# Optimization experiments

Hardware: AMD Instinct MI355X
Metric: run time of the kernel (lower is better)

Reference implementation:

```python
import jax, jax.numpy as jnp
import numpy as np

N_NODES = 10000
NUM_GENE = 2000
N_EDGES = 160000
HEADS = 10
HID = 128          # GAT layer1 out_channels
LATENT = 128
LOWER = 64
CLUSTERS = 15
SIGMA = 0.5
NEG_SLOPE = 0.2


def gat_conv(x, src, dst, W, a_src, a_dst, b, concat):
    """PyG GATConv (eval mode, self-loops already appended to src/dst).
    x: [N, Fin]; W: [Fin, H*D]; a_src/a_dst: [H, D]; b: [H*D] or [D]."""
    N = x.shape[0]
    H, D = a_src.shape
    h = (x @ W).reshape(N, H, D)                       # [N,H,D]
    e_s = jnp.einsum('nhd,hd->nh', h, a_src)           # [N,H]
    e_d = jnp.einsum('nhd,hd->nh', h, a_dst)
    alpha = jax.nn.leaky_relu(e_s[src] + e_d[dst], NEG_SLOPE)   # [E,H]
    m = jax.ops.segment_max(alpha, dst, num_segments=N)          # [N,H]
    p = jnp.exp(alpha - m[dst])
    s = jax.ops.segment_sum(p, dst, num_segments=N)
    w = p / s[dst]                                     # segment softmax [E,H]
    out = jax.ops.segment_sum(h[src] * w[:, :, None], dst, num_segments=N)  # [N,H,D]
    out = out.reshape(N, H * D) if concat else out.mean(axis=1)
    return out + b


def add_self_loops(edge_index, n):
    loop = jnp.arange(n, dtype=edge_index.dtype)
    src = jnp.concatenate([edge_index[0], loop])
    dst = jnp.concatenate([edge_index[1], loop])
    return src, dst


def setup_inputs() -> dict:
    key = jax.random.key(0)
    ks = jax.random.split(key, 20)
    g = lambda k, shape, fan: jax.random.normal(k, shape, jnp.float32) * (1.0 / np.sqrt(fan))
    inp = {
        'x': jax.random.normal(ks[0], (N_NODES, NUM_GENE), jnp.float32),
        'edge_index': jax.random.randint(ks[1], (2, N_EDGES), 0, N_NODES, dtype=jnp.int32),
        'noise': jax.random.normal(ks[2], (N_NODES, NUM_GENE), jnp.float32) * SIGMA,
        # GAT layer 1: in=NUM_GENE, out=HID, heads=HEADS, concat
        'W1': g(ks[3], (NUM_GENE, HEADS * HID), NUM_GENE),
        'a1_src': g(ks[4], (HEADS, HID), HID),
        'a1_dst': g(ks[5], (HEADS, HID), HID),
        'b1': jnp.zeros((HEADS * HID,), jnp.float32),
        # GAT layer 2: in=HEADS*HID, out=LATENT, heads=HEADS, mean
        'W2': g(ks[6], (HEADS * HID, HEADS * LATENT), HEADS * HID),
        'a2_src': g(ks[7], (HEADS, LATENT), LATENT),
        'a2_dst': g(ks[8], (HEADS, LATENT), LATENT),
        'b2': jnp.zeros((LATENT,), jnp.float32),
        # MLP
        'Wm1': g(ks[9], (NUM_GENE, LATENT), NUM_GENE),
        'bm1': jnp.zeros((LATENT,), jnp.float32),
        'Wm2': g(ks[10], (LATENT, LATENT), LATENT),
        'bm2': jnp.zeros((LATENT,), jnp.float32),
        # projection heads
        'Wf': g(ks[11], (LATENT, LOWER), LATENT),
        'bf': jnp.zeros((LOWER,), jnp.float32),
        'Wc': g(ks[12], (LATENT, CLUSTERS), LATENT),
        'bc': jnp.zeros((CLUSTERS,), jnp.float32),
    }
    return inp


def reference(x, edge_index, noise, W1, a1_src, a1_dst, b1, W2, a2_src, a2_dst, b2,
              Wm1, bm1, Wm2, bm2, Wf, bf, Wc, bc):
    N = x.shape[0]
    src, dst = add_self_loops(edge_index, N)

    # x_aug = x + F.normalize(noise, dim=1)
    nrm = jnp.sqrt(jnp.sum(noise * noise, axis=1, keepdims=True))
    x_aug = x + noise / jnp.maximum(nrm, 1e-12)

    def gat_enc(inp):
        h1 = jax.nn.relu(gat_conv(inp, src, dst, W1, a1_src, a1_dst, b1, concat=True))
        h2 = jax.nn.relu(gat_conv(h1, src, dst, W2, a2_src, a2_dst, b2, concat=False))
        return h2

    gx = gat_enc(x)          # [N, LATENT]
    gx1 = gat_enc(x_aug)
    gx2 = (jax.nn.relu(x @ Wm1 + bm1)) @ Wm2 + bm2   # MLP

    g0 = gx.mean(axis=0)     # global avg pooling -> [LATENT]
    g1 = gx1.mean(axis=0)
    g2 = gx2.mean(axis=0)

    T = 0.2
    e01 = jnp.exp(jnp.dot(g0, g1) / T)
    e02 = jnp.exp(jnp.dot(g0, g2) / T)
    e12 = jnp.exp(jnp.dot(g1, g2) / T)
    loss_graph = -jnp.log10(e01 / (e01 + e02 + e12))

    gx_node = gx @ Wf + bf
    gx1_node = gx1 @ Wf + bf
    gx2_node = gx2 @ Wf + bf
    gx_c = (gx @ Wc + bc).T      # [CLUSTERS, N]
    gx1_c = (gx1 @ Wc + bc).T
    return (gx_node, gx1_node, gx2_node, loss_graph, gx_c, gx1_c)
```

## Files before the change

### kernel.cpp

```cpp
#include <hip/hip_runtime.h>
#include <hip/hip_bf16.h>

#define N_NODESC 10000
#define M_PAD    10112
#define RT_TILES 79
#define NUM_GENE 2000
#define KPAD_G   2048
#define N_EDGESC 160000
#define E_TOT    170000
#define HEADS    10
#define F1       1280
#define LATENTC  128
#define LOWERC   64
#define CLUST    15

typedef __attribute__((ext_vector_type(8))) short   short8;
typedef __attribute__((ext_vector_type(4))) float   f32x4;
typedef __attribute__((ext_vector_type(4))) unsigned short ushort4_;

__device__ __forceinline__ float bf2f(unsigned short u){
    unsigned int x = ((unsigned int)u) << 16;
    return __builtin_bit_cast(float, x);
}
__device__ __forceinline__ unsigned short f2bf(float f){
    __hip_bfloat16 h = __float2bfloat16(f);
    return __builtin_bit_cast(unsigned short, h);
}
__device__ __forceinline__ void gload16(const void* g, void* l) {
    __builtin_amdgcn_global_load_lds((const __attribute__((address_space(1))) void*)g,
                                     (__attribute__((address_space(3))) void*)l, 16, 0, 0);
}

template<int OMODE, int FOLD>
__global__ __launch_bounds__(512, 2)
void gemm256(const unsigned short* __restrict__ A, int lda,
             const unsigned short* __restrict__ BT, int ldb,
             void* __restrict__ Cp, int ldc,
             int NK, int NT, int M_real,
             const float* __restrict__ mbias, unsigned short* __restrict__ mout)
{
    __shared__ short smem[65536];

    const int nwg = gridDim.x;
    const int q = nwg >> 3, r = nwg & 7;
    const int xcd = blockIdx.x & 7, idx = blockIdx.x >> 3;
    const int wgid = (xcd < r ? xcd * (q + 1) : r * (q + 1) + (xcd - r) * q) + idx;
    const int bm = wgid / NT, bn = wgid - bm * NT;

    const int t = threadIdx.x, w = t >> 6, lane = t & 63;
    const int wr2 = (w >> 2) * 64;
    const int wc2 = (w & 3) * 32;
    const int lrow = lane & 15, lq = lane >> 4;

    int rowc[2], swc[2], loff[2];
    #pragma unroll
    for (int cc = 0; cc < 2; ++cc) {
        int c = cc * 512 + t;
        int row = c >> 3, slot = c & 7;
        rowc[cc] = row;
        swc[cc]  = (slot ^ (row & 7)) << 3;
        loff[cc] = c * 8;
    }
    auto stageA = [&](int buf, int h, int kt) {
        short* dst = smem + buf * 32768 + h * 8192;
        const unsigned short* src = A + (size_t)(bm * 256 + h * 128) * lda + kt * 64;
        #pragma unroll
        for (int cc = 0; cc < 2; ++cc)
            gload16(src + (size_t)rowc[cc] * lda + swc[cc], dst + loff[cc]);
    };
    auto stageB = [&](int buf, int h, int kt) {
        short* dst = smem + buf * 32768 + 16384 + h * 8192;
        const unsigned short* src = BT + (size_t)(bn * 256 + h * 128) * ldb + kt * 64;
        #pragma unroll
        for (int cc = 0; cc < 2; ++cc)
            gload16(src + (size_t)rowc[cc] * ldb + swc[cc], dst + loff[cc]);
    };
    auto rdA = [&](int buf, int h, int mi, int ks) -> short8 {
        int r7 = wr2 + mi * 16 + lrow;
        return *(const short8*)(smem + buf * 32768 + h * 8192 + r7 * 64
                                + (((ks * 4 + lq) ^ (r7 & 7)) << 3));
    };
    auto rdB = [&](int buf, int h, int ni, int ks) -> short8 {
        int r7 = wc2 + ni * 16 + lrow;
        return *(const short8*)(smem + buf * 32768 + 16384 + h * 8192 + r7 * 64
                                + (((ks * 4 + lq) ^ (r7 & 7)) << 3));
    };

    f32x4 acc00[4][2] = {}, acc01[4][2] = {}, acc10[4][2] = {}, acc11[4][2] = {};
    short8 a0[4][2], a1[4][2], b0[2][2], b1[2][2];

    auto domfma = [&](f32x4 (&ac)[4][2], short8 (&aa)[4][2], short8 (&bb)[2][2]) {
        __builtin_amdgcn_s_setprio(1);
        #pragma unroll
        for (int mi = 0; mi < 4; ++mi)
            #pragma unroll
            for (int ni = 0; ni < 2; ++ni)
                #pragma unroll
                for (int ks = 0; ks < 2; ++ks)
                    ac[mi][ni] = __builtin_amdgcn_mfma_f32_16x16x32_bf16(
                        aa[mi][ks], bb[ni][ks], ac[mi][ni], 0, 0, 0);
        __builtin_amdgcn_s_setprio(0);
    };

    stageA(0, 0, 0); stageB(0, 0, 0); stageB(0, 1, 0); stageA(0, 1, 0);

    for (int kt = 0; kt < NK; ++kt) {
        const int buf = kt & 1, nbuf = buf ^ 1;
        const bool pf = (kt + 1 < NK);
        asm volatile("s_waitcnt vmcnt(4)" ::: "memory");
        __builtin_amdgcn_sched_barrier(0);
        __builtin_amdgcn_s_barrier();
        __builtin_amdgcn_sched_barrier(0);
        #pragma unroll
        for (int mi = 0; mi < 4; ++mi) { a0[mi][0] = rdA(buf, 0, mi, 0); a0[mi][1] = rdA(buf, 0, mi, 1); }
        #pragma unroll
        for (int ni = 0; ni < 2; ++ni) { b0[ni][0] = rdB(buf, 0, ni, 0); b0[ni][1] = rdB(buf, 0, ni, 1); }
        if (pf) stageA(nbuf, 0, kt + 1);
        domfma(acc00, a0, b0);
        if (pf) { asm volatile("s_waitcnt vmcnt(4)" ::: "memory"); }
        else    { asm volatile("s_waitcnt vmcnt(2)" ::: "memory"); }
        __builtin_amdgcn_sched_barrier(0);
        __builtin_amdgcn_s_barrier();
        __builtin_amdgcn_sched_barrier(0);
        #pragma unroll
        for (int ni = 0; ni < 2; ++ni) { b1[ni][0] = rdB(buf, 1, ni, 0); b1[ni][1] = rdB(buf, 1, ni, 1); }
        if (pf) stageB(nbuf, 0, kt + 1);
        domfma(acc01, a0, b1);
        if (pf) { asm volatile("s_waitcnt vmcnt(4)" ::: "memory"); }
        else    { asm volatile("s_waitcnt vmcnt(0)" ::: "memory"); }
        __builtin_amdgcn_sched_barrier(0);
        __builtin_amdgcn_s_barrier();
        __builtin_amdgcn_sched_barrier(0);
        #pragma unroll
        for (int mi = 0; mi < 4; ++mi) { a1[mi][0] = rdA(buf, 1, mi, 0); a1[mi][1] = rdA(buf, 1, mi, 1); }
        if (pf) stageB(nbuf, 1, kt + 1);
        domfma(acc10, a1, b0);
        if (pf) stageA(nbuf, 1, kt + 1);
        domfma(acc11, a1, b1);
    }

    const bool mlp_tile = FOLD && (bn == NT - 1);
    #pragma unroll
    for (int qa = 0; qa < 2; ++qa) {
        #pragma unroll
        for (int qb = 0; qb < 2; ++qb) {
            f32x4 (&ac)[4][2] = (qa == 0) ? (qb == 0 ? acc00 : acc01)
                                          : (qb == 0 ? acc10 : acc11);
            if (mlp_tile) {
                if (qb != 0) continue;
                #pragma unroll
                for (int mi = 0; mi < 4; ++mi) {
                    #pragma unroll
                    for (int ni = 0; ni < 2; ++ni) {
                        int col = wc2 + ni * 16 + lrow;
                        #pragma unroll
                        for (int qq = 0; qq < 4; ++qq) {
                            int grow = bm * 256 + qa * 128 + wr2 + mi * 16 + lq * 4 + qq;
                            if (grow < N_NODESC) {
                                float val = fmaxf(ac[mi][ni][qq] + mbias[col], 0.f);
                                mout[(size_t)grow * 128 + col] = f2bf(val);
                            }
                        }
                    }
                }
                continue;
            }
            #pragma unroll
            for (int mi = 0; mi < 4; ++mi) {
                #pragma unroll
                for (int ni = 0; ni < 2; ++ni) {
                    int gcol = bn * 256 + qb * 128 + wc2 + ni * 16 + lrow;
                    #pragma unroll
                    for (int qq = 0; qq < 4; ++qq) {
                        int grow = bm * 256 + qa * 128 + wr2 + mi * 16 + lq * 4 + qq;
                        float val = ac[mi][ni][qq];
                        int rslab = grow >= M_PAD ? grow - M_PAD : grow;
                        if (rslab >= M_real) val = 0.f;
                        if constexpr (OMODE == 0)
                            ((unsigned short*)Cp)[(size_t)grow * ldc + gcol] = f2bf(val);
                        else
                            ((float*)Cp)[(size_t)grow * ldc + gcol] = val;
                    }
                }
            }
        }
    }
}

template<int OMODE, int BIAS, int RELU>
__global__ __launch_bounds__(256)
void gemm2(const unsigned short* __restrict__ A, int lda,
           const unsigned short* __restrict__ BT, int ldb,
           const float* __restrict__ bias,
           void* __restrict__ Cp, int ldc,
           int KT, int NT, int M_real)
{
    __shared__ short smem[16384];

    const int nwg = gridDim.x;
    const int q = nwg >> 3, r = nwg & 7;
    const int xcd = blockIdx.x & 7, idx = blockIdx.x >> 3;
    const int wgid = (xcd < r ? xcd * (q + 1) : r * (q + 1) + (xcd - r) * q) + idx;
    const int bm = wgid / NT, bn = wgid - bm * NT;

    const int t = threadIdx.x, w = t >> 6, lane = t & 63;
    const int wr = (w >> 1) * 64, wc = (w & 1) * 64;
    const int lrow = lane & 15, lq = lane >> 4;

    const unsigned short* Ag[2];
    const unsigned short* Bg[2];
    int lds_off[2];
    #pragma unroll
    for (int cc = 0; cc < 2; ++cc) {
        int c = cc * 256 + t;
        int row = c >> 2, slot = c & 3;
        int gk = (slot ^ ((row >> 1) & 3)) << 3;
        Ag[cc] = A  + (size_t)(bm * 128 + row) * lda + gk;
        Bg[cc] = BT + (size_t)(bn * 128 + row) * ldb + gk;
        lds_off[cc] = cc * 2048 + w * 512 + lane * 8;
    }

    auto stage = [&](int buf, int kt) {
        const int kk = kt * 32;
        #pragma unroll
        for (int cc = 0; cc < 2; ++cc) {
            gload16(Ag[cc] + kk, smem + buf * 8192 + lds_off[cc]);
            gload16(Bg[cc] + kk, smem + buf * 8192 + 4096 + lds_off[cc]);
        }
    };

    f32x4 acc[4][4] = {};
    stage(0, 0);
    __syncthreads();
    int cur = 0;
    for (int kt = 0; kt < KT; ++kt) {
        if (kt + 1 < KT) stage(cur ^ 1, kt + 1);
        const short* As = smem + cur * 8192;
        const short* Bs = As + 4096;
        short8 af[4], bf_[4];
        #pragma unroll
        for (int mi = 0; mi < 4; ++mi) {
            int rr = wr + mi * 16 + lrow;
            af[mi] = *(const short8*)(&As[rr * 32 + ((lq ^ ((rr >> 1) & 3)) << 3)]);
        }
        #pragma unroll
        for (int ni = 0; ni < 4; ++ni) {
            int rr = wc + ni * 16 + lrow;
            bf_[ni] = *(const short8*)(&Bs[rr * 32 + ((lq ^ ((rr >> 1) & 3)) << 3)]);
        }
        #pragma unroll
        for (int mi = 0; mi < 4; ++mi)
            #pragma unroll
            for (int ni = 0; ni < 4; ++ni)
                acc[mi][ni] = __builtin_amdgcn_mfma_f32_16x16x32_bf16(af[mi], bf_[ni], acc[mi][ni], 0, 0, 0);
        __syncthreads();
        cur ^= 1;
    }

    #pragma unroll
    for (int mi = 0; mi < 4; ++mi) {
        #pragma unroll
        for (int ni = 0; ni < 4; ++ni) {
            int gcol = bn * 128 + wc + ni * 16 + lrow;
            #pragma unroll
            for (int qq = 0; qq < 4; ++qq) {
                int grow = bm * 128 + wr + mi * 16 + lq * 4 + qq;
                float val = acc[mi][ni][qq];
                if constexpr (BIAS) val += bias[gcol];
                if constexpr (RELU) val = fmaxf(val, 0.f);
                if (grow >= M_real) val = 0.f;
                ((float*)Cp)[(size_t)grow * ldc + gcol] = val;
            }
        }
    }
}

__global__ void convert_both_k(const float* __restrict__ x, const float* __restrict__ noise,
                               unsigned short* __restrict__ out)
{
    __shared__ float sred[4];
    __shared__ float srn;
    int row = blockIdx.x, t = threadIdx.x;
    int kc = t * 8;
    f32x4 n0 = {}, n1 = {};
    float ss = 0.f;
    if (t < 250) {
        n0 = *(const f32x4*)(noise + (size_t)row * NUM_GENE + kc);
        n1 = *(const f32x4*)(noise + (size_t)row * NUM_GENE + kc + 4);
        ss = n0.x*n0.x + n0.y*n0.y + n0.z*n0.z + n0.w*n0.w
           + n1.x*n1.x + n1.y*n1.y + n1.z*n1.z + n1.w*n1.w;
    }
    for (int off = 32; off; off >>= 1) ss += __shfl_down(ss, off);
    if ((t & 63) == 0) sred[t >> 6] = ss;
    __syncthreads();
    if (t == 0) srn = 1.f / fmaxf(sqrtf(sred[0] + sred[1] + sred[2] + sred[3]), 1e-12f);
    __syncthreads();
    if (t >= 250) return;
    float rn = srn;
    f32x4 a0 = *(const f32x4*)(x + (size_t)row * NUM_GENE + kc);
    f32x4 a1 = *(const f32x4*)(x + (size_t)row * NUM_GENE + kc + 4);
    short8 v0, v1;
    #pragma unroll
    for (int i = 0; i < 4; ++i) {
        v0[i]     = (short)f2bf(a0[i]);
        v0[4 + i] = (short)f2bf(a1[i]);
        v1[i]     = (short)f2bf(a0[i] + n0[i] * rn);
        v1[4 + i] = (short)f2bf(a1[i] + n1[i] * rn);
    }
    *(short8*)(out + (size_t)row * KPAD_G + kc) = v0;
    *(short8*)(out + (size_t)(M_PAD + row) * KPAD_G + kc) = v1;
}

__global__ void transpose_bf_k(const float* __restrict__ in, unsigned short* __restrict__ out,
                               int R, int C, int Kpad)
{
    __shared__ float tile[32][33];
    int tx = threadIdx.x & 31, ty = threadIdx.x >> 5;
    int c0 = blockIdx.x * 32, r0 = blockIdx.y * 32;
    #pragma unroll
    for (int i = 0; i < 4; ++i) {
        int r = r0 + ty + i * 8, c = c0 + tx;
        tile[ty + i * 8][tx] = (r < R && c < C) ? in[(size_t)r * C + c] : 0.f;
    }
    __syncthreads();
    #pragma unroll
    for (int i = 0; i < 4; ++i) {
        int c = c0 + ty + i * 8;
        int r = r0 + tx;
        if (c < C && r < Kpad) out[(size_t)c * Kpad + r] = f2bf(tile[tx][ty + i * 8]);
    }
}

__global__ void hist_k(const int* __restrict__ ei, int* __restrict__ cnt)
{
    int e = blockIdx.x * 256 + threadIdx.x;
    if (e >= E_TOT) return;
    int d = (e < N_EDGESC) ? ei[N_EDGESC + e] : (e - N_EDGESC);
    atomicAdd(&cnt[d], 1);
}

__global__ void scan_k(const int* __restrict__ cnt, int* __restrict__ rowp, int* __restrict__ cursor)
{
    __shared__ int buf[1024];
    int t = threadIdx.x;
    int loc[10];
    int s = 0, base = t * 10;
    #pragma unroll
    for (int i = 0; i < 10; ++i) {
        int idx = base + i;
        int v = (idx < N_NODESC) ? cnt[idx] : 0;
        loc[i] = v; s += v;
    }
    buf[t] = s; __syncthreads();
    for (int off = 1; off < 1024; off <<= 1) {
        int tmp = (t >= off) ? buf[t - off] : 0;
        __syncthreads();
        buf[t] += tmp;
        __syncthreads();
    }
    int run = buf[t] - s;
    #pragma unroll
    for (int i = 0; i < 10; ++i) {
        int idx = base + i;
        if (idx < N_NODESC) { rowp[idx] = run; cursor[idx] = run; run += loc[i]; }
    }
    if (t == 1023) rowp[N_NODESC] = buf[1023];
}

__global__ void scatter_k(const int* __restrict__ ei, int* __restrict__ cursor,
                          int* __restrict__ col_src, int* __restrict__ dst_of)
{
    int e = blockIdx.x * 256 + threadIdx.x;
    if (e >= E_TOT) return;
    int s, d;
    if (e < N_EDGESC) { s = ei[e]; d = ei[N_EDGESC + e]; } else { s = d = e - N_EDGESC; }
    int pos = atomicAdd(&cursor[d], 1);
    col_src[pos] = s;
    dst_of[pos] = d;
}

__global__ void escores2_k(const unsigned short* __restrict__ h,
                           const float* __restrict__ a_src, const float* __restrict__ a_dst,
                           float* __restrict__ e_s, float* __restrict__ e_d)
{
    int t = threadIdx.x;
    int half = (t >= 160);
    int tl = t - half * 160;
    int node2 = blockIdx.x * 2 + half;
    int p = node2 >= N_NODESC;
    int n = node2 - p * N_NODESC;
    int hh = tl >> 4, c = tl & 15;
    int off = hh * 128 + c * 8;
    short8 v = *(const short8*)(h + (size_t)(p * M_PAD + n) * F1 + off);
    float ps = 0.f, pd = 0.f;
    #pragma unroll
    for (int j = 0; j < 8; ++j) {
        float f = bf2f((unsigned short)v[j]);
        ps += f * a_src[off + j];
        pd += f * a_dst[off + j];
    }
    #pragma unroll
    for (int m = 1; m < 16; m <<= 1) {
        ps += __shfl_xor(ps, m, 16);
        pd += __shfl_xor(pd, m, 16);
    }
    if (c == 0) { e_s[node2 * HEADS + hh] = ps; e_d[node2 * HEADS + hh] = pd; }
}

__global__ void alpha_k(const int* __restrict__ colsrc, const int* __restrict__ dstof,
                        const float* __restrict__ e_s, const float* __restrict__ e_d,
                        float* __restrict__ alpha)
{
    int gid = blockIdx.x * 256 + threadIdx.x;
    if (gid >= 2 * E_TOT) return;
    int p = gid >= E_TOT;
    int e = gid - p * E_TOT;
    int s = colsrc[e], d = dstof[e];
    const float* er = e_s + (size_t)(p * N_NODESC + s) * HEADS;
    const float* dr = e_d + (size_t)(p * N_NODESC + d) * HEADS;
    #pragma unroll
    for (int h = 0; h < HEADS; ++h) {
        float a = er[h] + dr[h];
        a = a >= 0.f ? a : 0.2f * a;
        alpha[((size_t)p * HEADS + h) * E_TOT + e] = a;
    }
}

__global__ void nodems_k(const int* __restrict__ rowp, const float* __restrict__ alpha,
                         float2* __restrict__ minv)
{
    int gid = blockIdx.x * 256 + threadIdx.x;
    if (gid >= 2 * N_NODESC * HEADS) return;
    int p = gid >= N_NODESC * HEADS;
    int rr = gid - p * N_NODESC * HEADS;
    int n = rr / HEADS, hh = rr - n * HEADS;
    int beg = rowp[n], end = rowp[n + 1];
    const float* ap = alpha + ((size_t)p * HEADS + hh) * E_TOT;
    float m = -1e30f, ssum = 0.f;
    for (int e = beg; e < end; ++e) {
        float a = ap[e];
        if (a > m) { ssum = ssum * __expf(m - a) + 1.f; m = a; }
        else ssum += __expf(a - m);
    }
    float2 qo; qo.x = m; qo.y = 1.f / ssum;
    minv[gid] = qo;
}

__global__ void wexp_k(const int* __restrict__ dstof, const float2* __restrict__ minv,
                       float* __restrict__ alpha)
{
    int gid = blockIdx.x * 256 + threadIdx.x;
    if (gid >= 2 * E_TOT) return;
    int p = gid >= E_TOT;
    int e = gid - p * E_TOT;
    int d = dstof[e];
    const float2* mv = minv + (size_t)(p * N_NODESC + d) * HEADS;
    #pragma unroll
    for (int h = 0; h < HEADS; ++h) {
        float2 qv = mv[h];
        size_t o = ((size_t)p * HEADS + h) * E_TOT + e;
        alpha[o] = __expf(alpha[o] - qv.x) * qv.y;
    }
}

template<int L1MODE>
__global__ void agg_slice_k(const int* __restrict__ rowp, const int* __restrict__ colsrc,
                            const float* __restrict__ alpha,
                            const unsigned short* __restrict__ h,
                            const float* __restrict__ bias,
                            unsigned short* __restrict__ out)
{
    const int nwg = gridDim.x;
    const int q = nwg >> 3, r = nwg & 7;
    const int xcd = blockIdx.x & 7, idx = blockIdx.x >> 3;
    const int wgid = (xcd < r ? xcd * (q + 1) : r * (q + 1) + (xcd - r) * q) + idx;
    int ps = wgid / 625, nb = wgid - ps * 625;
    int p = ps / HEADS, s = ps - p * HEADS;
    int t = threadIdx.x;
    int nl = t >> 4, l16 = t & 15;
    int n = nb * 16 + nl;
    int beg = rowp[n], end = rowp[n + 1];
    const unsigned short* hb = h + (size_t)p * M_PAD * F1 + s * 128 + l16 * 8;
    const float* wb = alpha + ((size_t)p * HEADS + s) * E_TOT;
    float acc[8] = {};
    for (int e = beg; e < end; ++e) {
        int src = colsrc[e];
        float wv = wb[e];
        short8 rv = *(const short8*)(hb + (size_t)src * F1);
        #pragma unroll
        for (int j = 0; j < 8; ++j) acc[j] += wv * bf2f((unsigned short)rv[j]);
    }
    short8 o;
    if constexpr (L1MODE) {
        #pragma unroll
        for (int j = 0; j < 8; ++j)
            o[j] = (short)f2bf(fmaxf(acc[j] + bias[s * 128 + l16 * 8 + j], 0.f));
    } else {
        #pragma unroll
        for (int j = 0; j < 8; ++j) o[j] = (short)f2bf(acc[j]);
    }
    *(short8*)(out + (size_t)(p * M_PAD + n) * F1 + s * 128 + l16 * 8) = o;
}

__global__ void headmean_k(const unsigned short* __restrict__ tmp, const float* __restrict__ b2,
                           float* __restrict__ out)
{
    int gid = blockIdx.x * 256 + threadIdx.x;
    int pn = gid >> 4, d8 = (gid & 15) * 8;
    int p = pn >= N_NODESC;
    int n = pn - p * N_NODESC;
    const unsigned short* tp = tmp + (size_t)(p * M_PAD + n) * F1 + d8;
    float acc[8] = {};
    #pragma unroll
    for (int hh = 0; hh < HEADS; ++hh) {
        short8 v = *(const short8*)(tp + hh * 128);
        #pragma unroll
        for (int j = 0; j < 8; ++j) acc[j] += bf2f((unsigned short)v[j]);
    }
    float* op = out + (size_t)(p * M_PAD + n) * LATENTC + d8;
    #pragma unroll
    for (int j = 0; j < 8; ++j) op[j] = fmaxf(acc[j] * 0.1f + b2[d8 + j], 0.f);
}

__global__ void colsum_k(const float* __restrict__ g01, const float* __restrict__ g2,
                         float* __restrict__ gsum)
{
    int v = blockIdx.x / 40, b = blockIdx.x % 40;
    const float* src = (v == 0) ? g01 : (v == 1) ? g01 + (size_t)M_PAD * 128 : g2;
    int t = threadIdx.x, col = t & 127, ro = t >> 7;
    int rend = min((b + 1) * 250, N_NODESC);
    float acc = 0.f;
    for (int r = b * 250 + ro; r < rend; r += 2) acc += src[(size_t)r * 128 + col];
    __shared__ float part[256];
    part[t] = acc; __syncthreads();
    if (t < 128) atomicAdd(&gsum[v * 128 + col], part[t] + part[t + 128]);
}

__global__ void loss_k(const float* __restrict__ gsum, float* __restrict__ out)
{
    int t = threadIdx.x;
    float g0 = gsum[t] * 1e-4f, g1 = gsum[128 + t] * 1e-4f, g2 = gsum[256 + t] * 1e-4f;
    float d01 = g0 * g1, d02 = g0 * g2, d12 = g1 * g2;
    for (int off = 32; off; off >>= 1) {
        d01 += __shfl_down(d01, off); d02 += __shfl_down(d02, off); d12 += __shfl_down(d12, off);
    }
    __shared__ float s[3][2];
    if ((t & 63) == 0) { int w = t >> 6; s[0][w] = d01; s[1][w] = d02; s[2][w] = d12; }
    __syncthreads();
    if (t == 0) {
        float a01 = (s[0][0] + s[0][1]) * 5.f;
        float a02 = (s[1][0] + s[1][1]) * 5.f;
        float a12 = (s[2][0] + s[2][1]) * 5.f;
        float m = fmaxf(a01, fmaxf(a02, a12));
        float se = expf(a01 - m) + expf(a02 - m) + expf(a12 - m);
        *out = -((a01 - m) - logf(se)) / 2.302585092994046f;
    }
}

__global__ void proj_k(const float* __restrict__ g01, const float* __restrict__ g2,
                       const float* __restrict__ Wf, const float* __restrict__ bfv,
                       const float* __restrict__ Wc, const float* __restrict__ bc,
                       float* __restrict__ out)
{
    __shared__ float rowb[4][128];
    int m = blockIdx.y;
    const float* gx = (m == 0) ? g01 : (m == 1) ? g01 + (size_t)M_PAD * 128 : g2;
    float* out_node = out + (size_t)m * 640000;
    float* out_c = (m == 0) ? out + 1920001 : (m == 1) ? out + 2070001 : nullptr;
    int wid = threadIdx.x >> 6, l = threadIdx.x & 63;
    int n = blockIdx.x * 4 + wid;
    if (n >= N_NODESC) return;
    rowb[wid][l]      = gx[(size_t)n * 128 + l];
    rowb[wid][l + 64] = gx[(size_t)n * 128 + 64 + l];
    float acc = bfv[l];
    #pragma unroll 8
    for (int k = 0; k < 128; ++k) acc += rowb[wid][k] * Wf[k * 64 + l];
    out_node[(size_t)n * 64 + l] = acc;
    if (out_c != nullptr && l < CLUST) {
        float a2 = bc[l];
        #pragma unroll 8
        for (int k = 0; k < 128; ++k) a2 += rowb[wid][k] * Wc[k * CLUST + l];
        out_c[(size_t)l * N_NODESC + n] = a2;
    }
}

extern "C" void kernel_launch(void* const* d_in, const int* in_sizes, int n_in,
                              void* d_out, int out_size, void* d_ws, size_t ws_size,
                              hipStream_t stream)
{
    const float* x     = (const float*)d_in[0];
    const int*   ei    = (const int*)  d_in[1];
    const float* noise = (const float*)d_in[2];
    const float* W1    = (const float*)d_in[3];
    const float* a1s   = (const float*)d_in[4];
    const float* a1d   = (const float*)d_in[5];
    const float* b1    = (const float*)d_in[6];
    const float* W2    = (const float*)d_in[7];
    const float* a2s   = (const float*)d_in[8];
    const float* a2d   = (const float*)d_in[9];
    const float* b2    = (const float*)d_in[10];
    const float* Wm1   = (const float*)d_in[11];
    const float* bm1   = (const float*)d_in[12];
    const float* Wm2   = (const float*)d_in[13];
    const float* bm2   = (const float*)d_in[14];
    const float* Wf    = (const float*)d_in[15];
    const float* bfv   = (const float*)d_in[16];
    const float* Wc    = (const float*)d_in[17];
    const float* bc    = (const float*)d_in[18];
    float* out = (float*)d_out;

    size_t off = 0;
    auto alloc = [&](size_t bytes) { size_t o = off; off = (off + bytes + 255) & ~(size_t)255; return o; };
    char* ws = (char*)d_ws;
    unsigned short* xbuf2  = (unsigned short*)(ws + alloc((size_t)2 * M_PAD * KPAD_G * 2));
    unsigned short* hraw2  = (unsigned short*)(ws + alloc((size_t)2 * M_PAD * F1 * 2));
    unsigned short* w1t    = (unsigned short*)(ws + alloc((size_t)1536 * KPAD_G * 2));
    unsigned short* w2t    = (unsigned short*)(ws + alloc((size_t)F1 * F1 * 2));
    unsigned short* wm2t   = (unsigned short*)(ws + alloc((size_t)128 * 128 * 2));
    unsigned short* t_bf   = (unsigned short*)(ws + alloc((size_t)M_PAD * 128 * 2));
    float*  alpha  = (float*) (ws + alloc((size_t)2 * E_TOT * HEADS * 4));
    float2* minv   = (float2*)(ws + alloc((size_t)2 * N_NODESC * HEADS * 8));
    float*  es     = (float*) (ws + alloc((size_t)2 * N_NODESC * HEADS * 4));
    float*  edv    = (float*) (ws + alloc((size_t)2 * N_NODESC * HEADS * 4));
    int*    cnt    = (int*)   (ws + alloc((size_t)N_NODESC * 4));
    int*    rowp   = (int*)   (ws + alloc((size_t)(N_NODESC + 16) * 4));
    int*    cursor = (int*)   (ws + alloc((size_t)N_NODESC * 4));
    int*    colsrc = (int*)   (ws + alloc((size_t)E_TOT * 4));
    int*    dstof  = (int*)   (ws + alloc((size_t)E_TOT * 4));
    float*  gx01   = (float*) (ws + alloc((size_t)2 * M_PAD * 128 * 4));
    float*  gx2    = (float*) (ws + alloc((size_t)M_PAD * 128 * 4));
    float*  gsum   = (float*) (ws + alloc((size_t)384 * 4));
    unsigned short* h1x2 = xbuf2;
    unsigned short* tmp2 = xbuf2;
    (void)ws_size; (void)in_sizes; (void)n_in; (void)out_size;

    hipMemsetAsync(cnt, 0, (size_t)N_NODESC * 4, stream);
    hipMemsetAsync(gsum, 0, 384 * 4, stream);
    hipMemsetAsync(w1t + (size_t)1408 * KPAD_G, 0, (size_t)128 * KPAD_G * 2, stream);

    convert_both_k<<<N_NODESC, 256, 0, stream>>>(x, noise, xbuf2);

    transpose_bf_k<<<dim3(40, 64), 256, 0, stream>>>(W1,  w1t,  NUM_GENE, F1,  KPAD_G);
    transpose_bf_k<<<dim3(4, 64),  256, 0, stream>>>(Wm1, w1t + (size_t)1280 * KPAD_G, NUM_GENE, 128, KPAD_G);
    transpose_bf_k<<<dim3(40, 40), 256, 0, stream>>>(W2,  w2t,  F1,       F1,  F1);
    transpose_bf_k<<<dim3(4, 4),   256, 0, stream>>>(Wm2, wm2t, 128,      128, 128);

    hist_k   <<<(E_TOT + 255) / 256, 256, 0, stream>>>(ei, cnt);
    scan_k   <<<1, 1024, 0, stream>>>(cnt, rowp, cursor);
    scatter_k<<<(E_TOT + 255) / 256, 256, 0, stream>>>(ei, cursor, colsrc, dstof);

    gemm256<0,1><<<RT_TILES * 6, 512, 0, stream>>>(xbuf2, KPAD_G, w1t, KPAD_G,
        hraw2, F1, 32, 6, N_NODESC, bm1, t_bf);
    gemm2<1,1,0><<<RT_TILES, 256, 0, stream>>>(t_bf, 128, wm2t, 128,
        bm2, gx2, 128, 4, 1, N_NODESC);

    escores2_k<<<N_NODESC, 320, 0, stream>>>(hraw2, a1s, a1d, es, edv);
    alpha_k <<<(2 * E_TOT + 255) / 256, 256, 0, stream>>>(colsrc, dstof, es, edv, alpha);
    nodems_k<<<(2 * N_NODESC * HEADS + 255) / 256, 256, 0, stream>>>(rowp, alpha, minv);
    wexp_k  <<<(2 * E_TOT + 255) / 256, 256, 0, stream>>>(dstof, minv, alpha);
    agg_slice_k<1><<<12500, 256, 0, stream>>>(rowp, colsrc, alpha, hraw2, b1, h1x2);

    gemm256<0,0><<<RT_TILES * 5, 512, 0, stream>>>(h1x2, F1, w2t, F1,
        hraw2, F1, 20, 5, N_NODESC, nullptr, nullptr);
    escores2_k<<<N_NODESC, 320, 0, stream>>>(hraw2, a2s, a2d, es, edv);
    alpha_k <<<(2 * E_TOT + 255) / 256, 256, 0, stream>>>(colsrc, dstof, es, edv, alpha);
    nodems_k<<<(2 * N_NODESC * HEADS + 255) / 256, 256, 0, stream>>>(rowp, alpha, minv);
    wexp_k  <<<(2 * E_TOT + 255) / 256, 256, 0, stream>>>(dstof, minv, alpha);
    agg_slice_k<0><<<12500, 256, 0, stream>>>(rowp, colsrc, alpha, hraw2, nullptr, tmp2);
    headmean_k<<<1250, 256, 0, stream>>>(tmp2, b2, gx01);

    colsum_k<<<120, 256, 0, stream>>>(gx01, gx2, gsum);
    loss_k  <<<1, 128, 0, stream>>>(gsum, out + 1920000);

    proj_k<<<dim3(2500, 3), 256, 0, stream>>>(gx01, gx2, Wf, bfv, Wc, bc, out);
}
```

Baseline: 662.2 us.

## Restructure 256x256 GEMM into per-wave 128x64 tiles with k-half LDS staging

The 256x256 GEMM now gives each of its 8 waves one contiguous 128x64 output tile instead of four 64x32 quadrants. LDS staging splits each 64-wide K step into two 32-wide halves with a new XOR swizzle. Each wave loads 8 A fragments and 4 B fragments per half-step and issues 32 MFMAs, which gives more reuse per LDS read and fewer barriers per K step (two instead of three). The cost is a larger accumulator footprint (128 VGPRs of accumulators), which may hurt occupancy under launch_bounds(512,2) or cause spills.

After: 679.9 us. 2.7% more time.

```diff
diff --git a/kernel.cpp b/kernel.cpp
--- a/kernel.cpp
+++ b/kernel.cpp
@@ -48,61 +48,47 @@
     const int bm = wgid / NT, bn = wgid - bm * NT;
 
     const int t = threadIdx.x, w = t >> 6, lane = t & 63;
-    const int wr2 = (w >> 2) * 64;
-    const int wc2 = (w & 3) * 32;
+    const int wr = (w >> 2) * 128;
+    const int wc = (w & 3) * 64;
     const int lrow = lane & 15, lq = lane >> 4;
 
-    int rowc[2], swc[2], loff[2];
+    int rowc[2], kswz[2];
     #pragma unroll
     for (int cc = 0; cc < 2; ++cc) {
         int c = cc * 512 + t;
-        int row = c >> 3, slot = c & 7;
+        int row = c >> 2, slot = c & 3;
         rowc[cc] = row;
-        swc[cc]  = (slot ^ (row & 7)) << 3;
-        loff[cc] = c * 8;
-    }
-    auto stageA = [&](int buf, int h, int kt) {
-        short* dst = smem + buf * 32768 + h * 8192;
-        const unsigned short* src = A + (size_t)(bm * 256 + h * 128) * lda + kt * 64;
+        kswz[cc] = (slot ^ ((row >> 1) & 3)) << 3;
+    }
+    auto stageA = [&](int buf, int kh, int kt) {
+        short* dst = smem + buf * 16384 + kh * 8192;
+        const unsigned short* src = A + (size_t)(bm * 256) * lda + kt * 64 + kh * 32;
         #pragma unroll
         for (int cc = 0; cc < 2; ++cc)
-            gload16(src + (size_t)rowc[cc] * lda + swc[cc], dst + loff[cc]);
+            gload16(src + (size_t)rowc[cc] * lda + kswz[cc], dst + (cc * 512 + t) * 8);
     };
-    auto stageB = [&](int buf, int h, int kt) {
-        short* dst = smem + buf * 32768 + 16384 + h * 8192;
-        const unsigned short* src = BT + (size_t)(bn * 256 + h * 128) * ldb + kt * 64;
+    auto stageB = [&](int buf, int kh, int kt) {
+        short* dst = smem + 32768 + buf * 16384 + kh * 8192;
+        const unsigned short* src = BT + (size_t)(bn * 256) * ldb + kt * 64 + kh * 32;
         #pragma unroll
         for (int cc = 0; cc < 2; ++cc)
-            gload16(src + (size_t)rowc[cc] * ldb + swc[cc], dst + loff[cc]);
+            gload16(src + (size_t)rowc[cc] * ldb + kswz[cc], dst + (cc * 512 + t) * 8);
     };
-    auto rdA = [&](int buf, int h, int mi, int ks) -> short8 {
-        int r7 = wr2 + mi * 16 + lrow;
-        return *(const short8*)(smem + buf * 32768 + h * 8192 + r7 * 64
-                                + (((ks * 4 + lq) ^ (r7 & 7)) << 3));
+    auto rdA = [&](int buf, int mi, int ks) -> short8 {
+        int rr = wr + mi * 16 + lrow;
+        return *(const short8*)(smem + buf * 16384 + ks * 8192 + rr * 32
+                                + ((lq ^ ((rr >> 1) & 3)) << 3));
     };
-    auto rdB = [&](int buf, int h, int ni, int ks) -> short8 {
-        int r7 = wc2 + ni * 16 + lrow;
-        return *(const short8*)(smem + buf * 32768 + 16384 + h * 8192 + r7 * 64
-                                + (((ks * 4 + lq) ^ (r7 & 7)) << 3));
+    auto rdB = [&](int buf, int ni, int ks) -> short8 {
+        int rr = wc + ni * 16 + lrow;
+        return *(const short8*)(smem + 32768 + buf * 16384 + ks * 8192 + rr * 32
+                                + ((lq ^ ((rr >> 1) & 3)) << 3));
     };
 
-    f32x4 acc00[4][2] = {}, acc01[4][2] = {}, acc10[4][2] = {}, acc11[4][2] = {};
-    short8 a0[4][2], a1[4][2], b0[2][2], b1[2][2];
-
-    auto domfma = [&](f32x4 (&ac)[4][2], short8 (&aa)[4][2], short8 (&bb)[2][2]) {
-        __builtin_amdgcn_s_setprio(1);
-        #pragma unroll
-        for (int mi = 0; mi < 4; ++mi)
-            #pragma unroll
-            for (int ni = 0; ni < 2; ++ni)
-                #pragma unroll
-                for (int ks = 0; ks < 2; ++ks)
-                    ac[mi][ni] = __builtin_amdgcn_mfma_f32_16x16x32_bf16(
-                        aa[mi][ks], bb[ni][ks], ac[mi][ni], 0, 0, 0);
-        __builtin_amdgcn_s_setprio(0);
-    };
-
-    stageA(0, 0, 0); stageB(0, 0, 0); stageB(0, 1, 0); stageA(0, 1, 0);
+    f32x4 acc[8][4] = {};
+    short8 af[8], bf_[4];
+
+    stageA(0, 0, 0); stageB(0, 0, 0); stageA(0, 1, 0); stageB(0, 1, 0);
 
     for (int kt = 0; kt < NK; ++kt) {
         const int buf = kt & 1, nbuf = buf ^ 1;
@@ -112,76 +98,72 @@
         __builtin_amdgcn_s_barrier();
         __builtin_amdgcn_sched_barrier(0);
         #pragma unroll
-        for (int mi = 0; mi < 4; ++mi) { a0[mi][0] = rdA(buf, 0, mi, 0); a0[mi][1] = rdA(buf, 0, mi, 1); }
-        #pragma unroll
-        for (int ni = 0; ni < 2; ++ni) { b0[ni][0] = rdB(buf, 0, ni, 0); b0[ni][1] = rdB(buf, 0, ni, 1); }
-        if (pf) stageA(nbuf, 0, kt + 1);
-        domfma(acc00, a0, b0);
-        if (pf) { asm volatile("s_waitcnt vmcnt(4)" ::: "memory"); }
-        else    { asm volatile("s_waitcnt vmcnt(2)" ::: "memory"); }
-        __builtin_amdgcn_sched_barrier(0);
-        __builtin_amdgcn_s_barrier();
-        __builtin_amdgcn_sched_barrier(0);
-        #pragma unroll
-        for (int ni = 0; ni < 2; ++ni) { b1[ni][0] = rdB(buf, 1, ni, 0); b1[ni][1] = rdB(buf, 1, ni, 1); }
-        if (pf) stageB(nbuf, 0, kt + 1);
-        domfma(acc01, a0, b1);
+        for (int mi = 0; mi < 8; ++mi) af[mi] = rdA(buf, mi, 0);
+        #pragma unroll
+        for (int ni = 0; ni < 4; ++ni) bf_[ni] = rdB(buf, ni, 0);
+        if (pf) { stageA(nbuf, 0, kt + 1); stageB(nbuf, 0, kt + 1); }
+        __builtin_amdgcn_s_setprio(1);
+        #pragma unroll
+        for (int mi = 0; mi < 8; ++mi)
+            #pragma unroll
+            for (int ni = 0; ni < 4; ++ni)
+                acc[mi][ni] = __builtin_amdgcn_mfma_f32_16x16x32_bf16(af[mi], bf_[ni], acc[mi][ni], 0, 0, 0);
+        __builtin_amdgcn_s_setprio(0);
         if (pf) { asm volatile("s_waitcnt vmcnt(4)" ::: "memory"); }
         else    { asm volatile("s_waitcnt vmcnt(0)" ::: "memory"); }
         __builtin_amdgcn_sched_barrier(0);
         __builtin_amdgcn_s_barrier();
         __builtin_amdgcn_sched_barrier(0);
         #pragma unroll
-        for (int mi = 0; mi < 4; ++mi) { a1[mi][0] = rdA(buf, 1, mi, 0); a1[mi][1] = rdA(buf, 1, mi, 1); }
-        if (pf) stageB(nbuf, 1, kt + 1);
-        domfma(acc10, a1, b0);
-        if (pf) stageA(nbuf, 1, kt + 1);
-        domfma(acc11, a1, b1);
+        for (int mi = 0; mi < 8; ++mi) af[mi] = rdA(buf, mi, 1);
+        #pragma unroll
+        for (int ni = 0; ni < 4; ++ni) bf_[ni] = rdB(buf, ni, 1);
+        if (pf) { stageA(nbuf, 1, kt + 1); stageB(nbuf, 1, kt + 1); }
+        __builtin_amdgcn_s_setprio(1);
+        #pragma unroll
+        for (int mi = 0; mi < 8; ++mi)
+            #pragma unroll
+            for (int ni = 0; ni < 4; ++ni)
+                acc[mi][ni] = __builtin_amdgcn_mfma_f32_16x16x32_bf16(af[mi], bf_[ni], acc[mi][ni], 0, 0, 0);
+        __builtin_amdgcn_s_setprio(0);
     }
 
     const bool mlp_tile = FOLD && (bn == NT - 1);
-    #pragma unroll
-    for (int qa = 0; qa < 2; ++qa) {
-        #pragma unroll
-        for (int qb = 0; qb < 2; ++qb) {
-            f32x4 (&ac)[4][2] = (qa == 0) ? (qb == 0 ? acc00 : acc01)
-                                          : (qb == 0 ? acc10 : acc11);
-            if (mlp_tile) {
-                if (qb != 0) continue;
+    if (mlp_tile) {
+        if (wc < 128) {
+            #pragma unroll
+            for (int mi = 0; mi < 8; ++mi) {
                 #pragma unroll
-                for (int mi = 0; mi < 4; ++mi) {
+                for (int ni = 0; ni < 4; ++ni) {
+                    int col = wc + ni * 16 + lrow;
                     #pragma unroll
-                    for (int ni = 0; ni < 2; ++ni) {
-                        int col = wc2 + ni * 16 + lrow;
-                        #pragma unroll
-                        for (int qq = 0; qq < 4; ++qq) {
-                            int grow = bm * 256 + qa * 128 + wr2 + mi * 16 + lq * 4 + qq;
-                            if (grow < N_NODESC) {
-                                float val = fmaxf(ac[mi][ni][qq] + mbias[col], 0.f);
-                                mout[(size_t)grow * 128 + col] = f2bf(val);
-                            }
+                    for (int qq = 0; qq < 4; ++qq) {
+                        int grow = bm * 256 + wr + mi * 16 + lq * 4 + qq;
+                        if (grow < N_NODESC) {
+                            float val = fmaxf(acc[mi][ni][qq] + mbias[col], 0.f);
+                            mout[(size_t)grow * 128 + col] = f2bf(val);
                         }
                     }
                 }
-                continue;
             }
+        }
+        return;
+    }
+    #pragma unroll
+    for (int mi = 0; mi < 8; ++mi) {
+        #pragma unroll
+        for (int ni = 0; ni < 4; ++ni) {
+            int gcol = bn * 256 + wc + ni * 16 + lrow;
             #pragma unroll
-            for (int mi = 0; mi < 4; ++mi) {
-                #pragma unroll
-                for (int ni = 0; ni < 2; ++ni) {
-                    int gcol = bn * 256 + qb * 128 + wc2 + ni * 16 + lrow;
-                    #pragma unroll
-                    for (int qq = 0; qq < 4; ++qq) {
-                        int grow = bm * 256 + qa * 128 + wr2 + mi * 16 + lq * 4 + qq;
-                        float val = ac[mi][ni][qq];
-                        int rslab = grow >= M_PAD ? grow - M_PAD : grow;
-                        if (rslab >= M_real) val = 0.f;
-                        if constexpr (OMODE == 0)
-                            ((unsigned short*)Cp)[(size_t)grow * ldc + gcol] = f2bf(val);
-                        else
-                            ((float*)Cp)[(size_t)grow * ldc + gcol] = val;
-                    }
-                }
+            for (int qq = 0; qq < 4; ++qq) {
+                int grow = bm * 256 + wr + mi * 16 + lq * 4 + qq;
+                float val = acc[mi][ni][qq];
+                int rslab = grow >= M_PAD ? grow - M_PAD : grow;
+                if (rslab >= M_real) val = 0.f;
+                if constexpr (OMODE == 0)
+                    ((unsigned short*)Cp)[(size_t)grow * ldc + gcol] = f2bf(val);
+                else
+                    ((float*)Cp)[(size_t)grow * ldc + gcol] = val;
             }
         }
     }
```
